# Optimization experiments

Measured on AMD Instinct MI355X. Metric: run time of the kernel, lower is better.

The kernel has to match this reference:

```python
import jax, jax.numpy as jnp
import numpy as np

OUT, L, LPS, K = 256, 24, 6, 3          # classes, layers, layers_per_stack, kernel
RC, GC, SC, FC = 64, 128, 64, 80        # residual, gate, skip, feature channels
SCALES = (4, 4, 4, 4)                   # upsample scales, prod = 256 (hop size)
AUX = 2                                 # aux_context_window
B, T = 2, 16384
TF = T // int(np.prod(SCALES)) + 2 * AUX  # 68 mel frames fed in


def _conv1d(x, w, b=None, dilation=1, pad=(0, 0)):
    # x: (B,C,T), w: (O,C,K)
    y = jax.lax.conv_general_dilated(x, w, (1,), [pad], rhs_dilation=(dilation,),
                                     dimension_numbers=('NCH', 'OIH', 'NCH'))
    return y if b is None else y + b[None, :, None]


def _smooth(x, k):
    # depthwise-in-time smoothing: Conv2d(1,1,(1,Kk)) applied to (B,1,C,T)
    Bb, C, Tt = x.shape
    Kk = k.shape[0]
    y = jax.lax.conv_general_dilated(x.reshape(Bb * C, 1, Tt), k.reshape(1, 1, Kk),
                                     (1,), [(Kk // 2, Kk // 2)],
                                     dimension_numbers=('NCH', 'OIH', 'NCH'))
    return y.reshape(Bb, C, Tt)


def _wavenet(x, feature, first_W, first_b, conv_W, conv_b, cond_W,
             skip_W, skip_b, res_W, res_b, last1_W, last1_b, last2_W, last2_b,
             convin_W, up_K):
    # shift right by one (teacher forcing) then one-hot -> (B, OUT, T)
    xs = jnp.pad(x, ((0, 0), (1, 0)))[:, :-1]
    xoh = jax.nn.one_hot(xs, OUT, dtype=jnp.float32).transpose(0, 2, 1)

    # ConvInUpsampleNetwork: valid conv over aux context, then nearest-up + smooth
    f = _conv1d(feature, convin_W)  # (B, FC, TF - 2*AUX)
    for i, s in enumerate(SCALES):
        f = jnp.repeat(f, s, axis=-1)
        f = _smooth(f, up_K[i])
    # f: (B, FC, T)

    out = jnp.einsum('oc,bct->bot', first_W, xoh) + first_b[None, :, None]
    skips = jnp.zeros((x.shape[0], SC, x.shape[1]), jnp.float32)
    for l in range(L):
        d = 2 ** (l % LPS)
        pad = (K - 1) * d  # causal: left-pad only (== torch pad both + trim right)
        h = _conv1d(out, conv_W[l], conv_b[l], dilation=d, pad=(pad, 0))
        h = h + jnp.einsum('oc,bct->bot', cond_W[l], f)
        a, g = jnp.split(h, 2, axis=1)
        z = jnp.tanh(a) * jax.nn.sigmoid(g)  # (B, GC//2, T)
        skips = skips + jnp.einsum('oc,bct->bot', skip_W[l], z) + skip_b[l][None, :, None]
        out = jnp.einsum('oc,bct->bot', res_W[l], z) + res_b[l][None, :, None] + out
    h = jax.nn.relu(skips)
    h = jax.nn.relu(jnp.einsum('oc,bct->bot', last1_W, h) + last1_b[None, :, None])
    h = jnp.einsum('oc,bct->bot', last2_W, h) + last2_b[None, :, None]
    return h  # (B, OUT, T)


def setup_inputs() -> dict:
    key = jax.random.key(0)
    ks = jax.random.split(key, 12)
    s = 0.05
    return {
        'x': jax.random.randint(ks[0], (B, T), 0, OUT),
        'feature': jax.random.normal(ks[1], (B, FC, TF), jnp.float32),
        'first_W': jax.random.normal(ks[2], (RC, OUT), jnp.float32) * s,
        'first_b': jnp.zeros((RC,), jnp.float32),
        'conv_W': jax.random.normal(ks[3], (L, GC, RC, K), jnp.float32) * s,
        'conv_b': jnp.zeros((L, GC), jnp.float32),
        'cond_W': jax.random.normal(ks[4], (L, GC, FC), jnp.float32) * s,
        'skip_W': jax.random.normal(ks[5], (L, SC, GC // 2), jnp.float32) * s,
        'skip_b': jnp.zeros((L, SC), jnp.float32),
        'res_W': jax.random.normal(ks[6], (L, RC, GC // 2), jnp.float32) * s,
        'res_b': jnp.zeros((L, RC), jnp.float32),
        'last1_W': jax.random.normal(ks[7], (SC, SC), jnp.float32) * s,
        'last1_b': jnp.zeros((SC,), jnp.float32),
        'last2_W': jax.random.normal(ks[8], (OUT, SC), jnp.float32) * s,
        'last2_b': jnp.zeros((OUT,), jnp.float32),
        'convin_W': jax.random.normal(ks[9], (FC, FC, 2 * AUX + 1), jnp.float32) * s,
        'up_K': jnp.full((len(SCALES), 9), 1.0 / 9.0, jnp.float32),
    }


def reference(x, feature, first_W, first_b, conv_W, conv_b, cond_W,
              skip_W, skip_b, res_W, res_b, last1_W, last1_b, last2_W, last2_b,
              convin_W, up_K):
    return _wavenet(x, feature, first_W, first_b, conv_W, conv_b, cond_W,
                    skip_W, skip_b, res_W, res_b, last1_W, last1_b,
                    last2_W, last2_b, convin_W, up_K)
```

## Files before the change

### kernel.cpp

```cpp
#include <hip/hip_runtime.h>
#include <math.h>

#define T_LEN   16384
#define NB      2
#define FCH     80
#define NLAYERS 24
#define TFRAMES 68
#define PAD     76

typedef __attribute__((ext_vector_type(8))) short bf16x8;
typedef __attribute__((ext_vector_type(4))) float f32x4;

static __device__ inline unsigned short f2bf(float f) {
    unsigned int u = __float_as_uint(f);
    unsigned int r = (u + 0x7FFFu + ((u >> 16) & 1u)) >> 16;
    return (unsigned short)r;
}

__global__ void k_pack(const float* __restrict__ convW, const float* __restrict__ condW,
                       const float* __restrict__ skipW, const float* __restrict__ resW,
                       const float* __restrict__ last1W, const float* __restrict__ last2W,
                       const float* __restrict__ firstW, const float* __restrict__ firstb,
                       unsigned short* __restrict__ ATb, unsigned short* __restrict__ SRTb,
                       unsigned short* __restrict__ W1b, unsigned short* __restrict__ W2b,
                       float* __restrict__ firstWT) {
    int idx = blockIdx.x * 256 + threadIdx.x;
    const int nAT = NLAYERS * 128 * 288;
    const int nSR = NLAYERS * 128 * 64;
    const int e0 = nAT, e1 = e0 + nSR, e2 = e1 + 4096, e3 = e2 + 16384, e4 = e3 + 16384;
    if (idx < e0) {
        int k = idx % 288;
        int o = (idx / 288) & 127;
        int l = idx / (288 * 128);
        float v = 0.f;
        if (k < 192) v = convW[(((l * 128 + o) * 64) + (k & 63)) * 3 + (k >> 6)];
        else if (k - 192 < 80) v = condW[(l * 128 + o) * 80 + (k - 192)];
        ATb[idx] = f2bf(v);
    } else if (idx < e1) {
        int j = idx - e0;
        int k = j & 63;
        int o2 = (j >> 6) & 127;
        int l = j / (64 * 128);
        float v = (o2 < 64) ? skipW[(l * 64 + o2) * 64 + k]
                            : resW[(l * 64 + (o2 - 64)) * 64 + k];
        SRTb[j] = f2bf(v);
    } else if (idx < e2) {
        W1b[idx - e1] = f2bf(last1W[idx - e1]);
    } else if (idx < e3) {
        W2b[idx - e2] = f2bf(last2W[idx - e2]);
    } else if (idx < e4) {
        int j = idx - e3;
        int xs = j >> 6, c = j & 63;
        firstWT[j] = firstW[c * 256 + xs] + firstb[c];
    }
}

__global__ void k_convin(const float* __restrict__ feat, const float* __restrict__ W,
                         float* __restrict__ f0) {
    int idx = blockIdx.x * 256 + threadIdx.x;
    if (idx >= NB * FCH * 64) return;
    int t = idx & 63;
    int o = (idx >> 6) % FCH;
    int b = idx / (64 * FCH);
    const float* fb = feat + b * FCH * TFRAMES;
    const float* wo = W + o * FCH * 5;
    float acc = 0.f;
    for (int i = 0; i < FCH; ++i) {
        const float* fi = fb + i * TFRAMES + t;
        const float* wi = wo + i * 5;
#pragma unroll
        for (int k = 0; k < 5; ++k) acc += fi[k] * wi[k];
    }
    f0[idx] = acc;
}

__global__ void k_up(const float* __restrict__ in, float* __restrict__ out,
                     const float* __restrict__ kern, int Tin) {
    int Tout = Tin * 4;
    int idx = blockIdx.x * 256 + threadIdx.x;
    if (idx >= NB * FCH * Tout) return;
    int t = idx % Tout;
    int bc = idx / Tout;
    const float* ib = in + bc * Tin;
    float acc = 0.f;
#pragma unroll
    for (int k = 0; k < 9; ++k) {
        int u = t + k - 4;
        if (u >= 0 && u < Tout) acc += kern[k] * ib[u >> 2];
    }
    out[idx] = acc;
}

__global__ __launch_bounds__(256)
void k_up_last(const float* __restrict__ in, unsigned short* __restrict__ outH,
               const float* __restrict__ kern) {
    __shared__ float sF[18 * 80];
    const int tid = threadIdx.x;
    const int b  = blockIdx.x >> 8;
    const int t0 = (blockIdx.x & 255) * 64;
    const int fr0 = (t0 >> 2) - 1;

    for (int idx = tid; idx < 18 * 80; idx += 256) {
        int c = idx / 18, fr = idx - c * 18;
        int gfr = fr0 + fr;
        float v = 0.f;
        if (gfr >= 0 && gfr < 4096) v = in[((size_t)b * 80 + c) * 4096 + gfr];
        sF[fr * 80 + c] = v;
    }
    float kr[9];
#pragma unroll
    for (int k = 0; k < 9; ++k) kr[k] = kern[k];
    __syncthreads();

    for (int idx = tid; idx < 64 * 96; idx += 256) {
        int c = idx % 96;
        int t = idx / 96;
        float acc = 0.f;
        if (c < 80) {
            int ubase = t0 + t - 4;
#pragma unroll
            for (int k = 0; k < 9; ++k) {
                int fr = ((ubase + k) >> 2) - fr0;
                acc += kr[k] * sF[fr * 80 + c];
            }
        }
        outH[((size_t)b * T_LEN + t0 + t) * 96 + c] = f2bf(acc);
    }
}

__global__ __launch_bounds__(512, 1)
void k_stack(const int* __restrict__ x, const float* __restrict__ firstWT,
             const float* __restrict__ prevF, const unsigned short* __restrict__ prevH,
             float* __restrict__ nextF, unsigned short* __restrict__ nextH,
             float* __restrict__ skipF, const unsigned short* __restrict__ ffb,
             const unsigned short* __restrict__ ATb, const unsigned short* __restrict__ SRTb,
             const float* __restrict__ convB, const float* __restrict__ skipB,
             const float* __restrict__ resB,
             const unsigned short* __restrict__ W1b, const float* __restrict__ b1,
             const unsigned short* __restrict__ W2b, const float* __restrict__ b2,
             float* __restrict__ outp, int flags)
{
    __shared__ __align__(16) unsigned short s_P[264 * PAD];
    __shared__ __align__(16) unsigned short s_Z[256 * PAD];

    const int tid  = threadIdx.x;
    const int b    = blockIdx.x >> 7;
    const int t0   = (blockIdx.x & 127) * 128;
    const int lane = tid & 63;
    const int wv   = tid >> 6;
    const int col  = lane & 15;
    const int quad = lane >> 4;
    const int pair = wv & 3;
    const int par  = wv >> 2;
    const int chA  = 16 * pair + 4 * quad;
    const int srm  = (wv < 4) ? wv : (wv - 4);
    const int chS  = 16 * srm + 4 * quad;
    const bool firstStack = (flags & 1) != 0;
    const bool lastStack  = (flags & 2) != 0;

    const int ts_out[6] = {0, 0, 1, 2, 4, 8};

    for (int i = tid; i < 8 * (PAD / 2); i += 512) {
        int r = i / (PAD / 2), dw = i - r * (PAD / 2);
        ((unsigned int*)(s_P + r * PAD))[dw] = 0u;
    }
    if (firstStack) {
        for (int i = tid; i < 256 * 8; i += 512) {
            int r = i >> 3, seg = i & 7;
            int g = t0 - 128 + r;
            bf16x8 v = {0, 0, 0, 0, 0, 0, 0, 0};
            if (g >= 0) {
                int xs = (g == 0) ? 0 : x[b * T_LEN + g - 1];
                const float* p = firstWT + xs * 64 + seg * 8;
                f32x4 a0 = *(const f32x4*)p;
                f32x4 a1 = *(const f32x4*)(p + 4);
                v[0] = (short)f2bf(a0[0]); v[1] = (short)f2bf(a0[1]);
                v[2] = (short)f2bf(a0[2]); v[3] = (short)f2bf(a0[3]);
                v[4] = (short)f2bf(a1[0]); v[5] = (short)f2bf(a1[1]);
                v[6] = (short)f2bf(a1[2]); v[7] = (short)f2bf(a1[3]);
            }
            *(bf16x8*)(s_P + (8 + r) * PAD + seg * 8) = v;
        }
    } else {
        const unsigned short* hb = prevH + (size_t)b * T_LEN * 64;
        for (int i = tid; i < 256 * 8; i += 512) {
            int r = i >> 3, seg = i & 7;
            int g = t0 - 128 + r;
            bf16x8 v = {0, 0, 0, 0, 0, 0, 0, 0};
            if (g >= 0) v = *(const bf16x8*)(hb + (size_t)g * 64 + seg * 8);
            *(bf16x8*)(s_P + (8 + r) * PAD + seg * 8) = v;
        }
    }

    f32x4 resReg[8];
    f32x4 skipAcc[8];
#pragma unroll
    for (int i = 0; i < 8; ++i) skipAcc[i] = (f32x4){0.f, 0.f, 0.f, 0.f};
    if (wv >= 4) {
        if (firstStack) {
#pragma unroll
            for (int i = 0; i < 8; ++i) {
                int t = t0 + i * 16 + col;
                int xs = (t == 0) ? 0 : x[b * T_LEN + t - 1];
                resReg[i] = *(const f32x4*)(firstWT + xs * 64 + chS);
            }
        } else {
#pragma unroll
            for (int i = 0; i < 8; ++i)
                resReg[i] = *(const f32x4*)(prevF +
                              ((size_t)b * T_LEN + t0 + i * 16 + col) * 64 + chS);
        }
    }
    __syncthreads();

#pragma unroll 1
    for (int l = 0; l < 6; ++l) {
        const int d  = 1 << l;
        const int ts = ts_out[l];

        const unsigned short* AL = ATb + (size_t)l * 128 * 288;
        bf16x8 frA0[9], frA1[9];
#pragma unroll
        for (int ks = 0; ks < 9; ++ks) {
            frA0[ks] = *(const bf16x8*)(AL + (size_t)(16 * pair + col) * 288 + ks * 32 + quad * 8);
            frA1[ks] = *(const bf16x8*)(AL + (size_t)(64 + 16 * pair + col) * 288 + ks * 32 + quad * 8);
        }
        f32x4 cbA = *(const f32x4*)(convB + l * 128 + chA);
        f32x4 cbG = *(const f32x4*)(convB + l * 128 + 64 + chA);

#pragma unroll 1
        for (int tl = ts; tl < 16; ++tl) {
            if ((tl & 1) != par) continue;
            const int r_base = 8 + tl * 16 + col;
            int g = t0 - 128 + tl * 16 + col;
            int gcl = g < 0 ? 0 : g;
            const unsigned short* fc = ffb + ((size_t)b * T_LEN + gcl) * 96 + quad * 8;
            bf16x8 f6 = *(const bf16x8*)(fc);
            bf16x8 f7 = *(const bf16x8*)(fc + 32);
            bf16x8 f8 = *(const bf16x8*)(fc + 64);
            f32x4 a0 = (f32x4){0.f, 0.f, 0.f, 0.f};
            f32x4 a1 = (f32x4){0.f, 0.f, 0.f, 0.f};
#pragma unroll
            for (int ks = 0; ks < 6; ++ks) {
                int r_in = r_base - 2 * d + (ks >> 1) * d;
                bf16x8 fB = *(const bf16x8*)(s_P + r_in * PAD + (ks & 1) * 32 + quad * 8);
                a0 = __builtin_amdgcn_mfma_f32_16x16x32_bf16(frA0[ks], fB, a0, 0, 0, 0);
                a1 = __builtin_amdgcn_mfma_f32_16x16x32_bf16(frA1[ks], fB, a1, 0, 0, 0);
            }
            a0 = __builtin_amdgcn_mfma_f32_16x16x32_bf16(frA0[6], f6, a0, 0, 0, 0);
            a1 = __builtin_amdgcn_mfma_f32_16x16x32_bf16(frA1[6], f6, a1, 0, 0, 0);
            a0 = __builtin_amdgcn_mfma_f32_16x16x32_bf16(frA0[7], f7, a0, 0, 0, 0);
            a1 = __builtin_amdgcn_mfma_f32_16x16x32_bf16(frA1[7], f7, a1, 0, 0, 0);
            a0 = __builtin_amdgcn_mfma_f32_16x16x32_bf16(frA0[8], f8, a0, 0, 0, 0);
            a1 = __builtin_amdgcn_mfma_f32_16x16x32_bf16(frA1[8], f8, a1, 0, 0, 0);

            unsigned int pk[2];
#pragma unroll
            for (int r2 = 0; r2 < 2; ++r2) {
                float zz[2];
#pragma unroll
                for (int e = 0; e < 2; ++e) {
                    float av = a0[2 * r2 + e] + cbA[2 * r2 + e];
                    float gv = a1[2 * r2 + e] + cbG[2 * r2 + e];
                    float th = 1.f - 2.f * __builtin_amdgcn_rcpf(__expf(2.f * av) + 1.f);
                    float sg = __builtin_amdgcn_rcpf(1.f + __expf(-gv));
                    zz[e] = th * sg;
                }
                pk[r2] = (unsigned int)f2bf(zz[0]) | ((unsigned int)f2bf(zz[1]) << 16);
            }
            unsigned int* zp = (unsigned int*)(s_Z + (tl * 16 + col) * PAD + chA);
            zp[0] = pk[0];
            zp[1] = pk[1];
        }
        __syncthreads();

        const unsigned short* SL = SRTb + (size_t)l * 128 * 64;
        if (wv < 4) {
            bf16x8 wk0 = *(const bf16x8*)(SL + (size_t)(16 * srm + col) * 64 + quad * 8);
            bf16x8 wk1 = *(const bf16x8*)(SL + (size_t)(16 * srm + col) * 64 + 32 + quad * 8);
            f32x4 sb4 = *(const f32x4*)(skipB + l * 64 + chS);
#pragma unroll
            for (int i = 0; i < 8; ++i) {
                const int zr = ((8 + i) * 16 + col) * PAD;
                bf16x8 fz0 = *(const bf16x8*)(s_Z + zr + quad * 8);
                bf16x8 fz1 = *(const bf16x8*)(s_Z + zr + 32 + quad * 8);
                f32x4 s = (f32x4){0.f, 0.f, 0.f, 0.f};
                s = __builtin_amdgcn_mfma_f32_16x16x32_bf16(wk0, fz0, s, 0, 0, 0);
                s = __builtin_amdgcn_mfma_f32_16x16x32_bf16(wk1, fz1, s, 0, 0, 0);
#pragma unroll
                for (int e = 0; e < 4; ++e) skipAcc[i][e] += s[e] + sb4[e];
            }
        } else {
            bf16x8 wr0 = *(const bf16x8*)(SL + (size_t)(64 + 16 * srm + col) * 64 + quad * 8);
            bf16x8 wr1 = *(const bf16x8*)(SL + (size_t)(64 + 16 * srm + col) * 64 + 32 + quad * 8);
            f32x4 rb4 = *(const f32x4*)(resB + l * 64 + chS);
#pragma unroll 1
            for (int tl = ts; tl < 8; ++tl) {
                const int zr = (tl * 16 + col) * PAD;
                bf16x8 fz0 = *(const bf16x8*)(s_Z + zr + quad * 8);
                bf16x8 fz1 = *(const bf16x8*)(s_Z + zr + 32 + quad * 8);
                const int row = 8 + tl * 16 + col;
                unsigned int* pv = (unsigned int*)(s_P + row * PAD + chS);
                unsigned int w0 = pv[0], w1 = pv[1];
                f32x4 acc;
                acc[0] = __uint_as_float(w0 << 16);
                acc[1] = __uint_as_float(w0 & 0xFFFF0000u);
                acc[2] = __uint_as_float(w1 << 16);
                acc[3] = __uint_as_float(w1 & 0xFFFF0000u);
                acc = __builtin_amdgcn_mfma_f32_16x16x32_bf16(wr0, fz0, acc, 0, 0, 0);
                acc = __builtin_amdgcn_mfma_f32_16x16x32_bf16(wr1, fz1, acc, 0, 0, 0);
#pragma unroll
                for (int e = 0; e < 4; ++e) acc[e] += rb4[e];
                int g = t0 - 128 + tl * 16 + col;
                if (g < 0) acc = (f32x4){0.f, 0.f, 0.f, 0.f};
                pv[0] = (unsigned int)f2bf(acc[0]) | ((unsigned int)f2bf(acc[1]) << 16);
                pv[1] = (unsigned int)f2bf(acc[2]) | ((unsigned int)f2bf(acc[3]) << 16);
            }
            if (!(lastStack && l == 5)) {
#pragma unroll
                for (int i = 0; i < 8; ++i) {
                    const int zr = ((8 + i) * 16 + col) * PAD;
                    bf16x8 fz0 = *(const bf16x8*)(s_Z + zr + quad * 8);
                    bf16x8 fz1 = *(const bf16x8*)(s_Z + zr + 32 + quad * 8);
                    f32x4 acc = resReg[i];
                    acc = __builtin_amdgcn_mfma_f32_16x16x32_bf16(wr0, fz0, acc, 0, 0, 0);
                    acc = __builtin_amdgcn_mfma_f32_16x16x32_bf16(wr1, fz1, acc, 0, 0, 0);
#pragma unroll
                    for (int e = 0; e < 4; ++e) acc[e] += rb4[e];
                    resReg[i] = acc;
                    if (l < 5) {
                        const int row = 8 + (8 + i) * 16 + col;
                        unsigned int* qp = (unsigned int*)(s_P + row * PAD + chS);
                        qp[0] = (unsigned int)f2bf(acc[0]) | ((unsigned int)f2bf(acc[1]) << 16);
                        qp[1] = (unsigned int)f2bf(acc[2]) | ((unsigned int)f2bf(acc[3]) << 16);
                    }
                }
            }
        }
        __syncthreads();
    }

    if (!lastStack) {
        if (wv >= 4) {
#pragma unroll
            for (int i = 0; i < 8; ++i) {
                size_t base = ((size_t)b * T_LEN + t0 + i * 16 + col) * 64 + chS;
                *(f32x4*)(nextF + base) = resReg[i];
                unsigned int p01 = (unsigned int)f2bf(resReg[i][0]) | ((unsigned int)f2bf(resReg[i][1]) << 16);
                unsigned int p23 = (unsigned int)f2bf(resReg[i][2]) | ((unsigned int)f2bf(resReg[i][3]) << 16);
                unsigned int* hp = (unsigned int*)(nextH + base);
                hp[0] = p01;
                hp[1] = p23;
            }
        } else {
#pragma unroll
            for (int i = 0; i < 8; ++i) {
                size_t base = ((size_t)b * T_LEN + t0 + i * 16 + col) * 64 + chS;
                if (firstStack) {
                    *(f32x4*)(skipF + base) = skipAcc[i];
                } else {
                    f32x4 s = *(const f32x4*)(skipF + base);
#pragma unroll
                    for (int e = 0; e < 4; ++e) s[e] += skipAcc[i][e];
                    *(f32x4*)(skipF + base) = s;
                }
            }
        }
        return;
    }

    unsigned short* s_S = s_Z;
    unsigned short* s_H = s_Z + 128 * PAD;
    if (wv < 4) {
#pragma unroll
        for (int i = 0; i < 8; ++i) {
            size_t base = ((size_t)b * T_LEN + t0 + i * 16 + col) * 64 + chS;
            f32x4 s = *(const f32x4*)(skipF + base);
            float v0 = fmaxf(s[0] + skipAcc[i][0], 0.f);
            float v1 = fmaxf(s[1] + skipAcc[i][1], 0.f);
            float v2 = fmaxf(s[2] + skipAcc[i][2], 0.f);
            float v3 = fmaxf(s[3] + skipAcc[i][3], 0.f);
            unsigned int* sp = (unsigned int*)(s_S + (i * 16 + col) * PAD + chS);
            sp[0] = (unsigned int)f2bf(v0) | ((unsigned int)f2bf(v1) << 16);
            sp[1] = (unsigned int)f2bf(v2) | ((unsigned int)f2bf(v3) << 16);
        }
    }
    __syncthreads();

    {
        const int m1 = wv & 3;
        const int q1 = wv >> 2;
        bf16x8 fw0 = *(const bf16x8*)(W1b + (size_t)(16 * m1 + col) * 64 + quad * 8);
        bf16x8 fw1 = *(const bf16x8*)(W1b + (size_t)(16 * m1 + col) * 64 + 32 + quad * 8);
        f32x4 bb1 = *(const f32x4*)(b1 + 16 * m1 + 4 * quad);
#pragma unroll
        for (int i = 0; i < 8; ++i) {
            if ((i & 1) != q1) continue;
            const int zr = (i * 16 + col) * PAD;
            bf16x8 fz0 = *(const bf16x8*)(s_S + zr + quad * 8);
            bf16x8 fz1 = *(const bf16x8*)(s_S + zr + 32 + quad * 8);
            f32x4 a = (f32x4){0.f, 0.f, 0.f, 0.f};
            a = __builtin_amdgcn_mfma_f32_16x16x32_bf16(fw0, fz0, a, 0, 0, 0);
            a = __builtin_amdgcn_mfma_f32_16x16x32_bf16(fw1, fz1, a, 0, 0, 0);
            float h0 = fmaxf(a[0] + bb1[0], 0.f), h1 = fmaxf(a[1] + bb1[1], 0.f);
            float h2 = fmaxf(a[2] + bb1[2], 0.f), h3 = fmaxf(a[3] + bb1[3], 0.f);
            unsigned int* hp = (unsigned int*)(s_H + (i * 16 + col) * PAD + 16 * m1 + 4 * quad);
            hp[0] = (unsigned int)f2bf(h0) | ((unsigned int)f2bf(h1) << 16);
            hp[1] = (unsigned int)f2bf(h2) | ((unsigned int)f2bf(h3) << 16);
        }
    }
    __syncthreads();

#pragma unroll
    for (int p2 = 0; p2 < 2; ++p2) {
        const int m2 = wv + 8 * p2;
        bf16x8 fw0 = *(const bf16x8*)(W2b + (size_t)(16 * m2 + col) * 64 + quad * 8);
        bf16x8 fw1 = *(const bf16x8*)(W2b + (size_t)(16 * m2 + col) * 64 + 32 + quad * 8);
        f32x4 bb2 = *(const f32x4*)(b2 + 16 * m2 + 4 * quad);
#pragma unroll
        for (int i = 0; i < 8; ++i) {
            const int zr = (i * 16 + col) * PAD;
            bf16x8 fz0 = *(const bf16x8*)(s_H + zr + quad * 8);
            bf16x8 fz1 = *(const bf16x8*)(s_H + zr + 32 + quad * 8);
            f32x4 a = (f32x4){0.f, 0.f, 0.f, 0.f};
            a = __builtin_amdgcn_mfma_f32_16x16x32_bf16(fw0, fz0, a, 0, 0, 0);
            a = __builtin_amdgcn_mfma_f32_16x16x32_bf16(fw1, fz1, a, 0, 0, 0);
            int t = t0 + i * 16 + col;
            int o0 = 16 * m2 + 4 * quad;
#pragma unroll
            for (int e = 0; e < 4; ++e)
                outp[((size_t)b * 256 + o0 + e) * T_LEN + t] = a[e] + bb2[e];
        }
    }
}

extern "C" void kernel_launch(void* const* d_in, const int* in_sizes, int n_in,
                              void* d_out, int out_size, void* d_ws, size_t ws_size,
                              hipStream_t stream) {
    const int*   x       = (const int*)  d_in[0];
    const float* feature = (const float*)d_in[1];
    const float* firstW  = (const float*)d_in[2];
    const float* firstb  = (const float*)d_in[3];
    const float* convW   = (const float*)d_in[4];
    const float* convB   = (const float*)d_in[5];
    const float* condW   = (const float*)d_in[6];
    const float* skipW   = (const float*)d_in[7];
    const float* skipB   = (const float*)d_in[8];
    const float* resW    = (const float*)d_in[9];
    const float* resB    = (const float*)d_in[10];
    const float* last1W  = (const float*)d_in[11];
    const float* last1b  = (const float*)d_in[12];
    const float* last2W  = (const float*)d_in[13];
    const float* last2b  = (const float*)d_in[14];
    const float* convinW = (const float*)d_in[15];
    const float* upK     = (const float*)d_in[16];

    float* ws = (float*)d_ws;
    float* f0      = ws;
    float* f1      = f0 + 10240;
    float* f2      = f1 + 40960;
    float* f3      = f2 + 163840;
    float* firstWT = f3 + 655360;
    float* resA    = firstWT + 16384;
    float* resB_   = resA + 2097152;
    float* skipF   = resB_ + 2097152;
    unsigned short* mirA = (unsigned short*)(skipF + 2097152);
    unsigned short* mirB = mirA + 2097152;
    unsigned short* ffb  = mirB + 2097152;
    unsigned short* ATb  = ffb + 3145728;
    unsigned short* SRTb = ATb + 884736;
    unsigned short* W1b  = SRTb + 196608;
    unsigned short* W2b  = W1b + 4096;

    int n;
    n = NLAYERS * 128 * 288 + NLAYERS * 128 * 64 + 4096 + 16384 + 16384;
    k_pack<<<(n + 255) / 256, 256, 0, stream>>>(convW, condW, skipW, resW, last1W, last2W,
                                                firstW, firstb, ATb, SRTb, W1b, W2b, firstWT);
    n = NB * FCH * 64;
    k_convin<<<(n + 255) / 256, 256, 0, stream>>>(feature, convinW, f0);
    k_up<<<(NB * FCH * 256 + 255) / 256, 256, 0, stream>>>(f0, f1, upK + 0, 64);
    k_up<<<(NB * FCH * 1024 + 255) / 256, 256, 0, stream>>>(f1, f2, upK + 9, 256);
    k_up<<<(NB * FCH * 4096 + 255) / 256, 256, 0, stream>>>(f2, f3, upK + 18, 1024);
    k_up_last<<<NB * 256, 256, 0, stream>>>(f3, ffb, upK + 27);

    float* poF = resA;          float* pnF = resB_;
    unsigned short* poH = mirA; unsigned short* pnH = mirB;
    for (int s = 0; s < 4; ++s) {
        int flags = (s == 0 ? 1 : 0) | (s == 3 ? 2 : 0);
        k_stack<<<NB * 128, 512, 0, stream>>>(
            x, firstWT, poF, poH, pnF, pnH, skipF, ffb,
            ATb + (size_t)s * 6 * 128 * 288, SRTb + (size_t)s * 6 * 128 * 64,
            convB + s * 6 * 128, skipB + s * 6 * 64, resB + s * 6 * 64,
            W1b, last1b, W2b, last2b, (float*)d_out, flags);
        float* tf = poF; poF = pnF; pnF = tf;
        unsigned short* th = poH; poH = pnH; pnH = th;
    }
}
```

Measured before the change: 399.5 us.

## Double k_stack to 1024 threads, stage conditioning features in LDS, stream weights

```diff
diff --git a/kernel.cpp b/kernel.cpp
--- a/kernel.cpp
+++ b/kernel.cpp
@@ -7,6 +7,7 @@
 #define NLAYERS 24
 #define TFRAMES 68
 #define PAD     76
+#define FPAD    104
 
 typedef __attribute__((ext_vector_type(8))) short bf16x8;
 typedef __attribute__((ext_vector_type(4))) float f32x4;
@@ -128,7 +129,7 @@
     }
 }
 
-__global__ __launch_bounds__(512, 1)
+__global__ __launch_bounds__(1024, 1)
 void k_stack(const int* __restrict__ x, const float* __restrict__ firstWT,
              const float* __restrict__ prevF, const unsigned short* __restrict__ prevH,
              float* __restrict__ nextF, unsigned short* __restrict__ nextH,
@@ -142,6 +143,7 @@
 {
     __shared__ __align__(16) unsigned short s_P[264 * PAD];
     __shared__ __align__(16) unsigned short s_Z[256 * PAD];
+    __shared__ __align__(16) unsigned short s_F[256 * FPAD];
 
     const int tid  = threadIdx.x;
     const int b    = blockIdx.x >> 7;
@@ -151,21 +153,24 @@
     const int col  = lane & 15;
     const int quad = lane >> 4;
     const int pair = wv & 3;
-    const int par  = wv >> 2;
+    const int q1   = wv >> 2;
+    const int sub  = wv & 7;
+    const int m    = sub & 3;
+    const int h    = sub >> 2;
+    const int role = wv >> 3;
     const int chA  = 16 * pair + 4 * quad;
-    const int srm  = (wv < 4) ? wv : (wv - 4);
-    const int chS  = 16 * srm + 4 * quad;
+    const int chS  = 16 * m + 4 * quad;
     const bool firstStack = (flags & 1) != 0;
     const bool lastStack  = (flags & 2) != 0;
 
     const int ts_out[6] = {0, 0, 1, 2, 4, 8};
 
-    for (int i = tid; i < 8 * (PAD / 2); i += 512) {
+    for (int i = tid; i < 8 * (PAD / 2); i += 1024) {
         int r = i / (PAD / 2), dw = i - r * (PAD / 2);
         ((unsigned int*)(s_P + r * PAD))[dw] = 0u;
     }
     if (firstStack) {
-        for (int i = tid; i < 256 * 8; i += 512) {
+        for (int i = tid; i < 256 * 8; i += 1024) {
             int r = i >> 3, seg = i & 7;
             int g = t0 - 128 + r;
             bf16x8 v = {0, 0, 0, 0, 0, 0, 0, 0};
@@ -183,7 +188,7 @@
         }
     } else {
         const unsigned short* hb = prevH + (size_t)b * T_LEN * 64;
-        for (int i = tid; i < 256 * 8; i += 512) {
+        for (int i = tid; i < 256 * 8; i += 1024) {
             int r = i >> 3, seg = i & 7;
             int g = t0 - 128 + r;
             bf16x8 v = {0, 0, 0, 0, 0, 0, 0, 0};
@@ -191,24 +196,34 @@
             *(bf16x8*)(s_P + (8 + r) * PAD + seg * 8) = v;
         }
     }
-
-    f32x4 resReg[8];
-    f32x4 skipAcc[8];
-#pragma unroll
-    for (int i = 0; i < 8; ++i) skipAcc[i] = (f32x4){0.f, 0.f, 0.f, 0.f};
-    if (wv >= 4) {
+    {
+        const unsigned short* fb = ffb + (size_t)b * T_LEN * 96;
+        for (int i = tid; i < 256 * 12; i += 1024) {
+            int r = i / 12, seg = i - r * 12;
+            int g = t0 - 128 + r;
+            int gcl = g < 0 ? 0 : g;
+            *(bf16x8*)(s_F + r * FPAD + seg * 8) =
+                *(const bf16x8*)(fb + (size_t)gcl * 96 + seg * 8);
+        }
+    }
+
+    f32x4 resReg[4];
+    f32x4 skipAcc[4];
+#pragma unroll
+    for (int i = 0; i < 4; ++i) skipAcc[i] = (f32x4){0.f, 0.f, 0.f, 0.f};
+    if (role == 1) {
         if (firstStack) {
 #pragma unroll
-            for (int i = 0; i < 8; ++i) {
-                int t = t0 + i * 16 + col;
+            for (int i = 0; i < 4; ++i) {
+                int t = t0 + (4 * h + i) * 16 + col;
                 int xs = (t == 0) ? 0 : x[b * T_LEN + t - 1];
                 resReg[i] = *(const f32x4*)(firstWT + xs * 64 + chS);
             }
         } else {
 #pragma unroll
-            for (int i = 0; i < 8; ++i)
+            for (int i = 0; i < 4; ++i)
                 resReg[i] = *(const f32x4*)(prevF +
-                              ((size_t)b * T_LEN + t0 + i * 16 + col) * 64 + chS);
+                              ((size_t)b * T_LEN + t0 + (4 * h + i) * 16 + col) * 64 + chS);
         }
     }
     __syncthreads();
@@ -219,69 +234,69 @@
         const int ts = ts_out[l];
 
         const unsigned short* AL = ATb + (size_t)l * 128 * 288;
-        bf16x8 frA0[9], frA1[9];
-#pragma unroll
-        for (int ks = 0; ks < 9; ++ks) {
-            frA0[ks] = *(const bf16x8*)(AL + (size_t)(16 * pair + col) * 288 + ks * 32 + quad * 8);
-            frA1[ks] = *(const bf16x8*)(AL + (size_t)(64 + 16 * pair + col) * 288 + ks * 32 + quad * 8);
-        }
+        const size_t roA = (size_t)(16 * pair + col) * 288 + quad * 8;
+        const size_t roG = roA + (size_t)64 * 288;
         f32x4 cbA = *(const f32x4*)(convB + l * 128 + chA);
         f32x4 cbG = *(const f32x4*)(convB + l * 128 + 64 + chA);
 
 #pragma unroll 1
-        for (int tl = ts; tl < 16; ++tl) {
-            if ((tl & 1) != par) continue;
-            const int r_base = 8 + tl * 16 + col;
-            int g = t0 - 128 + tl * 16 + col;
-            int gcl = g < 0 ? 0 : g;
-            const unsigned short* fc = ffb + ((size_t)b * T_LEN + gcl) * 96 + quad * 8;
-            bf16x8 f6 = *(const bf16x8*)(fc);
-            bf16x8 f7 = *(const bf16x8*)(fc + 32);
-            bf16x8 f8 = *(const bf16x8*)(fc + 64);
+        for (int j = 0; j < 4; ++j) {
+            const int tl = q1 + 4 * j;
+            const bool v = tl >= ts;
+            const int tlc = v ? tl : ts;
+            const int r_base = 8 + tlc * 16 + col;
             f32x4 a0 = (f32x4){0.f, 0.f, 0.f, 0.f};
             f32x4 a1 = (f32x4){0.f, 0.f, 0.f, 0.f};
 #pragma unroll
             for (int ks = 0; ks < 6; ++ks) {
-                int r_in = r_base - 2 * d + (ks >> 1) * d;
-                bf16x8 fB = *(const bf16x8*)(s_P + r_in * PAD + (ks & 1) * 32 + quad * 8);
-                a0 = __builtin_amdgcn_mfma_f32_16x16x32_bf16(frA0[ks], fB, a0, 0, 0, 0);
-                a1 = __builtin_amdgcn_mfma_f32_16x16x32_bf16(frA1[ks], fB, a1, 0, 0, 0);
-            }
-            a0 = __builtin_amdgcn_mfma_f32_16x16x32_bf16(frA0[6], f6, a0, 0, 0, 0);
-            a1 = __builtin_amdgcn_mfma_f32_16x16x32_bf16(frA1[6], f6, a1, 0, 0, 0);
-            a0 = __builtin_amdgcn_mfma_f32_16x16x32_bf16(frA0[7], f7, a0, 0, 0, 0);
-            a1 = __builtin_amdgcn_mfma_f32_16x16x32_bf16(frA1[7], f7, a1, 0, 0, 0);
-            a0 = __builtin_amdgcn_mfma_f32_16x16x32_bf16(frA0[8], f8, a0, 0, 0, 0);
-            a1 = __builtin_amdgcn_mfma_f32_16x16x32_bf16(frA1[8], f8, a1, 0, 0, 0);
-
-            unsigned int pk[2];
-#pragma unroll
-            for (int r2 = 0; r2 < 2; ++r2) {
-                float zz[2];
-#pragma unroll
-                for (int e = 0; e < 2; ++e) {
-                    float av = a0[2 * r2 + e] + cbA[2 * r2 + e];
-                    float gv = a1[2 * r2 + e] + cbG[2 * r2 + e];
-                    float th = 1.f - 2.f * __builtin_amdgcn_rcpf(__expf(2.f * av) + 1.f);
-                    float sg = __builtin_amdgcn_rcpf(1.f + __expf(-gv));
-                    zz[e] = th * sg;
+                bf16x8 wa = *(const bf16x8*)(AL + roA + ks * 32);
+                bf16x8 wg = *(const bf16x8*)(AL + roG + ks * 32);
+                const int off = (ks & 1) * 32 + quad * 8;
+                const int r_in = r_base - 2 * d + (ks >> 1) * d;
+                bf16x8 fB = *(const bf16x8*)(s_P + r_in * PAD + off);
+                a0 = __builtin_amdgcn_mfma_f32_16x16x32_bf16(wa, fB, a0, 0, 0, 0);
+                a1 = __builtin_amdgcn_mfma_f32_16x16x32_bf16(wg, fB, a1, 0, 0, 0);
+            }
+#pragma unroll
+            for (int ks = 6; ks < 9; ++ks) {
+                bf16x8 wa = *(const bf16x8*)(AL + roA + ks * 32);
+                bf16x8 wg = *(const bf16x8*)(AL + roG + ks * 32);
+                bf16x8 fF = *(const bf16x8*)(s_F + (tlc * 16 + col) * FPAD
+                                             + (ks - 6) * 32 + quad * 8);
+                a0 = __builtin_amdgcn_mfma_f32_16x16x32_bf16(wa, fF, a0, 0, 0, 0);
+                a1 = __builtin_amdgcn_mfma_f32_16x16x32_bf16(wg, fF, a1, 0, 0, 0);
+            }
+            if (v) {
+                unsigned int pk[2];
+#pragma unroll
+                for (int r2 = 0; r2 < 2; ++r2) {
+                    float zz[2];
+#pragma unroll
+                    for (int e = 0; e < 2; ++e) {
+                        float av = a0[2 * r2 + e] + cbA[2 * r2 + e];
+                        float gv = a1[2 * r2 + e] + cbG[2 * r2 + e];
+                        float th = 1.f - 2.f * __builtin_amdgcn_rcpf(__expf(2.f * av) + 1.f);
+                        float sg = __builtin_amdgcn_rcpf(1.f + __expf(-gv));
+                        zz[e] = th * sg;
+                    }
+                    pk[r2] = (unsigned int)f2bf(zz[0]) | ((unsigned int)f2bf(zz[1]) << 16);
                 }
-                pk[r2] = (unsigned int)f2bf(zz[0]) | ((unsigned int)f2bf(zz[1]) << 16);
-            }
-            unsigned int* zp = (unsigned int*)(s_Z + (tl * 16 + col) * PAD + chA);
-            zp[0] = pk[0];
-            zp[1] = pk[1];
+                unsigned int* zp = (unsigned int*)(s_Z + (tl * 16 + col) * PAD + chA);
+                zp[0] = pk[0];
+                zp[1] = pk[1];
+            }
         }
         __syncthreads();
 
         const unsigned short* SL = SRTb + (size_t)l * 128 * 64;
-        if (wv < 4) {
-            bf16x8 wk0 = *(const bf16x8*)(SL + (size_t)(16 * srm + col) * 64 + quad * 8);
-            bf16x8 wk1 = *(const bf16x8*)(SL + (size_t)(16 * srm + col) * 64 + 32 + quad * 8);
+        if (role == 0) {
+            bf16x8 wk0 = *(const bf16x8*)(SL + (size_t)(16 * m + col) * 64 + quad * 8);
+            bf16x8 wk1 = *(const bf16x8*)(SL + (size_t)(16 * m + col) * 64 + 32 + quad * 8);
             f32x4 sb4 = *(const f32x4*)(skipB + l * 64 + chS);
 #pragma unroll
-            for (int i = 0; i < 8; ++i) {
-                const int zr = ((8 + i) * 16 + col) * PAD;
+            for (int i = 0; i < 4; ++i) {
+                const int gt = 8 + 4 * h + i;
+                const int zr = (gt * 16 + col) * PAD;
                 bf16x8 fz0 = *(const bf16x8*)(s_Z + zr + quad * 8);
                 bf16x8 fz1 = *(const bf16x8*)(s_Z + zr + 32 + quad * 8);
                 f32x4 s = (f32x4){0.f, 0.f, 0.f, 0.f};
@@ -291,11 +306,12 @@
                 for (int e = 0; e < 4; ++e) skipAcc[i][e] += s[e] + sb4[e];
             }
         } else {
-            bf16x8 wr0 = *(const bf16x8*)(SL + (size_t)(64 + 16 * srm + col) * 64 + quad * 8);
-            bf16x8 wr1 = *(const bf16x8*)(SL + (size_t)(64 + 16 * srm + col) * 64 + 32 + quad * 8);
+            bf16x8 wr0 = *(const bf16x8*)(SL + (size_t)(64 + 16 * m + col) * 64 + quad * 8);
+            bf16x8 wr1 = *(const bf16x8*)(SL + (size_t)(64 + 16 * m + col) * 64 + 32 + quad * 8);
             f32x4 rb4 = *(const f32x4*)(resB + l * 64 + chS);
-#pragma unroll 1
-            for (int tl = ts; tl < 8; ++tl) {
+#pragma unroll
+            for (int tl = 0; tl < 8; ++tl) {
+                if (tl < ts || (tl & 1) != h) continue;
                 const int zr = (tl * 16 + col) * PAD;
                 bf16x8 fz0 = *(const bf16x8*)(s_Z + zr + quad * 8);
                 bf16x8 fz1 = *(const bf16x8*)(s_Z + zr + 32 + quad * 8);
@@ -318,8 +334,9 @@
             }
             if (!(lastStack && l == 5)) {
 #pragma unroll
-                for (int i = 0; i < 8; ++i) {
-                    const int zr = ((8 + i) * 16 + col) * PAD;
+                for (int i = 0; i < 4; ++i) {
+                    const int gt = 8 + 4 * h + i;
+                    const int zr = (gt * 16 + col) * PAD;
                     bf16x8 fz0 = *(const bf16x8*)(s_Z + zr + quad * 8);
                     bf16x8 fz1 = *(const bf16x8*)(s_Z + zr + 32 + quad * 8);
                     f32x4 acc = resReg[i];
@@ -329,7 +346,7 @@
                     for (int e = 0; e < 4; ++e) acc[e] += rb4[e];
                     resReg[i] = acc;
                     if (l < 5) {
-                        const int row = 8 + (8 + i) * 16 + col;
+                        const int row = 8 + gt * 16 + col;
                         unsigned int* qp = (unsigned int*)(s_P + row * PAD + chS);
                         qp[0] = (unsigned int)f2bf(acc[0]) | ((unsigned int)f2bf(acc[1]) << 16);
                         qp[1] = (unsigned int)f2bf(acc[2]) | ((unsigned int)f2bf(acc[3]) << 16);
@@ -341,10 +358,10 @@
     }
 
     if (!lastStack) {
-        if (wv >= 4) {
-#pragma unroll
-            for (int i = 0; i < 8; ++i) {
-                size_t base = ((size_t)b * T_LEN + t0 + i * 16 + col) * 64 + chS;
+        if (role == 1) {
+#pragma unroll
+            for (int i = 0; i < 4; ++i) {
+                size_t base = ((size_t)b * T_LEN + t0 + (4 * h + i) * 16 + col) * 64 + chS;
                 *(f32x4*)(nextF + base) = resReg[i];
                 unsigned int p01 = (unsigned int)f2bf(resReg[i][0]) | ((unsigned int)f2bf(resReg[i][1]) << 16);
                 unsigned int p23 = (unsigned int)f2bf(resReg[i][2]) | ((unsigned int)f2bf(resReg[i][3]) << 16);
@@ -354,8 +371,8 @@
             }
         } else {
 #pragma unroll
-            for (int i = 0; i < 8; ++i) {
-                size_t base = ((size_t)b * T_LEN + t0 + i * 16 + col) * 64 + chS;
+            for (int i = 0; i < 4; ++i) {
+                size_t base = ((size_t)b * T_LEN + t0 + (4 * h + i) * 16 + col) * 64 + chS;
                 if (firstStack) {
                     *(f32x4*)(skipF + base) = skipAcc[i];
                 } else {
@@ -371,16 +388,17 @@
 
     unsigned short* s_S = s_Z;
     unsigned short* s_H = s_Z + 128 * PAD;
-    if (wv < 4) {
-#pragma unroll
-        for (int i = 0; i < 8; ++i) {
-            size_t base = ((size_t)b * T_LEN + t0 + i * 16 + col) * 64 + chS;
+    if (role == 0) {
+#pragma unroll
+        for (int i = 0; i < 4; ++i) {
+            const int lt = 4 * h + i;
+            size_t base = ((size_t)b * T_LEN + t0 + lt * 16 + col) * 64 + chS;
             f32x4 s = *(const f32x4*)(skipF + base);
             float v0 = fmaxf(s[0] + skipAcc[i][0], 0.f);
             float v1 = fmaxf(s[1] + skipAcc[i][1], 0.f);
             float v2 = fmaxf(s[2] + skipAcc[i][2], 0.f);
             float v3 = fmaxf(s[3] + skipAcc[i][3], 0.f);
-            unsigned int* sp = (unsigned int*)(s_S + (i * 16 + col) * PAD + chS);
+            unsigned int* sp = (unsigned int*)(s_S + (lt * 16 + col) * PAD + chS);
             sp[0] = (unsigned int)f2bf(v0) | ((unsigned int)f2bf(v1) << 16);
             sp[1] = (unsigned int)f2bf(v2) | ((unsigned int)f2bf(v3) << 16);
         }
@@ -389,14 +407,13 @@
 
     {
         const int m1 = wv & 3;
-        const int q1 = wv >> 2;
         bf16x8 fw0 = *(const bf16x8*)(W1b + (size_t)(16 * m1 + col) * 64 + quad * 8);
         bf16x8 fw1 = *(const bf16x8*)(W1b + (size_t)(16 * m1 + col) * 64 + 32 + quad * 8);
         f32x4 bb1 = *(const f32x4*)(b1 + 16 * m1 + 4 * quad);
 #pragma unroll
-        for (int i = 0; i < 8; ++i) {
-            if ((i & 1) != q1) continue;
-            const int zr = (i * 16 + col) * PAD;
+        for (int cc2 = 0; cc2 < 2; ++cc2) {
+            const int cc = q1 + 4 * cc2;
+            const int zr = (cc * 16 + col) * PAD;
             bf16x8 fz0 = *(const bf16x8*)(s_S + zr + quad * 8);
             bf16x8 fz1 = *(const bf16x8*)(s_S + zr + 32 + quad * 8);
             f32x4 a = (f32x4){0.f, 0.f, 0.f, 0.f};
@@ -404,28 +421,27 @@
             a = __builtin_amdgcn_mfma_f32_16x16x32_bf16(fw1, fz1, a, 0, 0, 0);
             float h0 = fmaxf(a[0] + bb1[0], 0.f), h1 = fmaxf(a[1] + bb1[1], 0.f);
             float h2 = fmaxf(a[2] + bb1[2], 0.f), h3 = fmaxf(a[3] + bb1[3], 0.f);
-            unsigned int* hp = (unsigned int*)(s_H + (i * 16 + col) * PAD + 16 * m1 + 4 * quad);
+            unsigned int* hp = (unsigned int*)(s_H + (cc * 16 + col) * PAD + 16 * m1 + 4 * quad);
             hp[0] = (unsigned int)f2bf(h0) | ((unsigned int)f2bf(h1) << 16);
             hp[1] = (unsigned int)f2bf(h2) | ((unsigned int)f2bf(h3) << 16);
         }
     }
     __syncthreads();
 
-#pragma unroll
-    for (int p2 = 0; p2 < 2; ++p2) {
-        const int m2 = wv + 8 * p2;
+    {
+        const int m2 = wv;
         bf16x8 fw0 = *(const bf16x8*)(W2b + (size_t)(16 * m2 + col) * 64 + quad * 8);
         bf16x8 fw1 = *(const bf16x8*)(W2b + (size_t)(16 * m2 + col) * 64 + 32 + quad * 8);
         f32x4 bb2 = *(const f32x4*)(b2 + 16 * m2 + 4 * quad);
 #pragma unroll
-        for (int i = 0; i < 8; ++i) {
-            const int zr = (i * 16 + col) * PAD;
+        for (int cc = 0; cc < 8; ++cc) {
+            const int zr = (cc * 16 + col) * PAD;
             bf16x8 fz0 = *(const bf16x8*)(s_H + zr + quad * 8);
             bf16x8 fz1 = *(const bf16x8*)(s_H + zr + 32 + quad * 8);
             f32x4 a = (f32x4){0.f, 0.f, 0.f, 0.f};
             a = __builtin_amdgcn_mfma_f32_16x16x32_bf16(fw0, fz0, a, 0, 0, 0);
             a = __builtin_amdgcn_mfma_f32_16x16x32_bf16(fw1, fz1, a, 0, 0, 0);
-            int t = t0 + i * 16 + col;
+            int t = t0 + cc * 16 + col;
             int o0 = 16 * m2 + 4 * quad;
 #pragma unroll
             for (int e = 0; e < 4; ++e)
@@ -487,7 +503,7 @@
     unsigned short* poH = mirA; unsigned short* pnH = mirB;
     for (int s = 0; s < 4; ++s) {
         int flags = (s == 0 ? 1 : 0) | (s == 3 ? 2 : 0);
-        k_stack<<<NB * 128, 512, 0, stream>>>(
+        k_stack<<<NB * 128, 1024, 0, stream>>>(
             x, firstWT, poF, poH, pnF, pnH, skipF, ffb,
             ATb + (size_t)s * 6 * 128 * 288, SRTb + (size_t)s * 6 * 128 * 64,
             convB + s * 6 * 128, skipB + s * 6 * 64, resB + s * 6 * 64,
```

New measurement: 497.2 us. +24.4%, slower.
